# Kernel optimization log

Measured on AMD Instinct MI355X. Metric: run time of the kernel, lower is better.

## Reference

```python
import jax, jax.numpy as jnp
import numpy as np

SOS = 1  # start-of-sequence token id (module references a global SOS)
VOCAB, EMBED, HIDDEN = 32000, 512, 1024

def setup_inputs() -> dict:
    key = jax.random.key(0)
    ks = jax.random.split(key, 8)
    B = 32
    s = lambda k, shape, scale: jax.random.normal(k, shape, dtype=jnp.float32) * scale
    return {
        "init_hidden": s(ks[0], (1, B, HIDDEN), 1.0),
        "encoder_outputs": s(ks[1], (B, 64, HIDDEN), 1.0),
        "tgt_len": 64,
        "embedding": s(ks[2], (VOCAB, EMBED), 1.0),
        "w_ih": s(ks[3], (3 * HIDDEN, EMBED), 0.03),
        "b_ih": s(ks[4], (3 * HIDDEN,), 0.03),
        "w_hh": s(ks[5], (3 * HIDDEN, HIDDEN), 0.03),
        "b_hh": s(ks[6], (3 * HIDDEN,), 0.03),
        "w_out": s(ks[7], (VOCAB, HIDDEN), 0.03),
        "b_out": jnp.zeros((VOCAB,), dtype=jnp.float32),
    }

def reference(init_hidden, encoder_outputs, tgt_len, embedding, w_ih, b_ih, w_hh, b_hh, w_out, b_out):
    B = init_hidden.shape[1]
    h0 = init_hidden[0]                       # [B, H] (num_layers=1)
    tok0 = jnp.full((B,), SOS, dtype=jnp.int32)

    def step(carry, _):
        h, tok = carry
        x = jnp.tanh(embedding[tok])          # [B, E]
        gi = x @ w_ih.T + b_ih                # [B, 3H]
        gh = h @ w_hh.T + b_hh                # [B, 3H]
        i_r, i_z, i_n = jnp.split(gi, 3, axis=-1)
        h_r, h_z, h_n = jnp.split(gh, 3, axis=-1)
        r = jax.nn.sigmoid(i_r + h_r)
        z = jax.nn.sigmoid(i_z + h_z)
        n = jnp.tanh(i_n + r * h_n)
        h_new = (1.0 - z) * n + z * h         # [B, H]
        logp = jax.nn.log_softmax(h_new @ w_out.T + b_out, axis=-1)  # [B, V]
        tok_new = jnp.argmax(logp, axis=-1).astype(jnp.int32)
        return (h_new, tok_new), logp

    (_, _), outputs = jax.lax.scan(step, (h0, tok0), None, length=tgt_len)
    return outputs                            # [T, B, V] log-probs (matches list of squeezed outputs)
```

## Files before the change

kernel.cpp:

```cpp
#include <hip/hip_runtime.h>
#include <math.h>

#define B    32
#define H    1024
#define EMB  512
#define V    32000
#define SOS  1

#define OFF_X   0
#define OFF_HA  16384
#define OFF_HB  49152
#define OFF_P   81920
#define OFF_C   113920
#define OFF_HHI 115968
#define OFF_HLO 132352
#define OFF_WHI 148736
#define OFF_WLO 16532736

#define NEG_INF (-3.0e38f)

typedef float f4v   __attribute__((ext_vector_type(4)));
typedef short short8v __attribute__((ext_vector_type(8)));
typedef float f32x4 __attribute__((ext_vector_type(4)));

#define MF(a,b,c) c = __builtin_amdgcn_mfma_f32_16x16x32_bf16(a, b, c, 0, 0, 0)

__device__ __forceinline__ unsigned short rnb(float x) {
    unsigned u = __float_as_uint(x);
    unsigned r = u + 0x7FFFu + ((u >> 16) & 1u);
    return (unsigned short)(r >> 16);
}
__device__ __forceinline__ float bfh(unsigned short s) {
    return __uint_as_float(((unsigned)s) << 16);
}
__device__ __forceinline__ void sm_merge(float& m, float& l, int& a,
                                         float om, float ol, int oa)
{
    const bool take = (om > m) || (om == m && oa < a);
    const float mn = take ? om : m;
    const int   an = take ? oa : a;
    l = l * expf(m - mn) + ol * expf(om - mn);
    m = mn; a = an;
}

__global__ void k_init(const float* __restrict__ ih, const float* __restrict__ emb,
                       const float* __restrict__ wout, float* __restrict__ ws)
{
    const size_t idx = (size_t)blockIdx.x * blockDim.x + threadIdx.x;
    const size_t stride = (size_t)gridDim.x * blockDim.x;
    for (size_t i = idx; i < EMB * B; i += stride)
        ws[OFF_X + i] = tanhf(emb[(size_t)SOS * EMB + (i >> 5)]);
    for (size_t i = idx; i < H * B; i += stride) {
        int j = (int)(i >> 5), b = (int)(i & 31);
        ws[OFF_HA + j * 32 + b] = ih[(size_t)b * H + j];
    }
    short* Whi = (short*)(ws + OFF_WHI);
    short* Wlo = (short*)(ws + OFF_WLO);
    for (size_t i = idx; i < (size_t)V * H; i += stride) {
        const float x = wout[i];
        const unsigned short hi = rnb(x);
        Whi[i] = (short)hi;
        Wlo[i] = (short)rnb(x - bfh(hi));
    }
}

__global__ __launch_bounds__(1024) void k_gru(
    const float* __restrict__ xG, const float* __restrict__ hold,
    const float* __restrict__ wih, const float* __restrict__ bih,
    const float* __restrict__ whh, const float* __restrict__ bhh,
    float* __restrict__ hnew, short* __restrict__ Hhi, short* __restrict__ Hlo)
{
    const int t   = threadIdx.x;
    const int blk = blockIdx.x;
    __shared__ float sred[4 * 1152];

    const int ks = t >> 7;
    const int pl = t & 127;
    const int p  = blk * 128 + pl;
    const int b  = p & 31;
    const int j  = p >> 5;

    float ar = 0.f, az = 0.f, ain = 0.f, ahn = 0.f;
    const int k0 = ks * 192, k1 = k0 + 192;

    const int xe = (k1 < EMB) ? k1 : EMB;
    for (int k = k0; k < xe; k += 4) {
        const float u0 = xG[(k + 0) * 32 + b];
        const float u1 = xG[(k + 1) * 32 + b];
        const float u2 = xG[(k + 2) * 32 + b];
        const float u3 = xG[(k + 3) * 32 + b];
        const float4 w0 = *(const float4*)&wih[(size_t)(0 * H + j) * EMB + k];
        const float4 w1 = *(const float4*)&wih[(size_t)(1 * H + j) * EMB + k];
        const float4 w2 = *(const float4*)&wih[(size_t)(2 * H + j) * EMB + k];
        ar  = fmaf(w0.x, u0, fmaf(w0.y, u1, fmaf(w0.z, u2, fmaf(w0.w, u3, ar))));
        az  = fmaf(w1.x, u0, fmaf(w1.y, u1, fmaf(w1.z, u2, fmaf(w1.w, u3, az))));
        ain = fmaf(w2.x, u0, fmaf(w2.y, u1, fmaf(w2.z, u2, fmaf(w2.w, u3, ain))));
    }
    const int hs = (k0 > EMB) ? k0 : EMB;
    for (int k = hs; k < k1; k += 4) {
        const int kh = k - EMB;
        const float u0 = hold[(kh + 0) * 32 + b];
        const float u1 = hold[(kh + 1) * 32 + b];
        const float u2 = hold[(kh + 2) * 32 + b];
        const float u3 = hold[(kh + 3) * 32 + b];
        const float4 w0 = *(const float4*)&whh[(size_t)(0 * H + j) * H + kh];
        const float4 w1 = *(const float4*)&whh[(size_t)(1 * H + j) * H + kh];
        const float4 w2 = *(const float4*)&whh[(size_t)(2 * H + j) * H + kh];
        ar  = fmaf(w0.x, u0, fmaf(w0.y, u1, fmaf(w0.z, u2, fmaf(w0.w, u3, ar))));
        az  = fmaf(w1.x, u0, fmaf(w1.y, u1, fmaf(w1.z, u2, fmaf(w1.w, u3, az))));
        ahn = fmaf(w2.x, u0, fmaf(w2.y, u1, fmaf(w2.z, u2, fmaf(w2.w, u3, ahn))));
    }

    sred[0 * 1152 + pl * 9 + ks] = ar;
    sred[1 * 1152 + pl * 9 + ks] = az;
    sred[2 * 1152 + pl * 9 + ks] = ain;
    sred[3 * 1152 + pl * 9 + ks] = ahn;
    __syncthreads();

    if (t < 128) {
        const int pp = blk * 128 + t;
        const int bb = pp & 31, jj = pp >> 5;
        float s0 = 0.f, s1 = 0.f, s2 = 0.f, s3 = 0.f;
#pragma unroll
        for (int q = 0; q < 8; ++q) {
            s0 += sred[0 * 1152 + t * 9 + q];
            s1 += sred[1 * 1152 + t * 9 + q];
            s2 += sred[2 * 1152 + t * 9 + q];
            s3 += sred[3 * 1152 + t * 9 + q];
        }
        float gr  = s0 + bih[jj]         + bhh[jj];
        float gz  = s1 + bih[H + jj]     + bhh[H + jj];
        float gin = s2 + bih[2 * H + jj];
        float ghn = s3 + bhh[2 * H + jj];
        float r = 1.f / (1.f + expf(-gr));
        float z = 1.f / (1.f + expf(-gz));
        float n = tanhf(gin + r * ghn);
        const int hidx = jj * 32 + bb;
        const float hv = (1.f - z) * n + z * hold[hidx];
        hnew[hidx] = hv;
        const unsigned short hi = rnb(hv);
        const unsigned short lo = rnb(hv - bfh(hi));
        const int pidx = (((jj >> 3) * 32) + bb) * 8 + (jj & 7);
        Hhi[pidx] = (short)hi;
        Hlo[pidx] = (short)lo;
    }
}

__global__ __launch_bounds__(256) void k_proj(
    const short* __restrict__ Whi, const short* __restrict__ Wlo,
    const short* __restrict__ Hhi, const short* __restrict__ Hlo,
    const float* __restrict__ bout, float* __restrict__ orow,
    float4* __restrict__ P)
{
    __shared__ float Dt[32 * 132];
    __shared__ float bl[128];
    __shared__ float pm[4][32], pls[4][32];
    __shared__ int   pa[4][32];

    const int t   = threadIdx.x;
    const int blk = blockIdx.x;
    const int r0  = blk * 128;
    const int w   = t >> 6;
    const int l   = t & 63;
    const int lr  = l & 15;
    const int lg  = l >> 4;

    if (t < 128) bl[t] = bout[r0 + t];

    const short* pAh = Whi + (size_t)(r0 + w * 32 + lr) * H + lg * 8;
    const short* pAl = Wlo + (size_t)(r0 + w * 32 + lr) * H + lg * 8;
    const short* pBh = Hhi + (lg * 32 + lr) * 8;
    const short* pBl = Hlo + (lg * 32 + lr) * 8;

    f32x4 acc00 = {0.f, 0.f, 0.f, 0.f};
    f32x4 acc01 = {0.f, 0.f, 0.f, 0.f};
    f32x4 acc10 = {0.f, 0.f, 0.f, 0.f};
    f32x4 acc11 = {0.f, 0.f, 0.f, 0.f};

#pragma unroll 4
    for (int c = 0; c < 32; ++c) {
        const short8v a0h = *(const short8v*)(pAh + c * 32);
        const short8v a1h = *(const short8v*)(pAh + 16 * H + c * 32);
        const short8v a0l = *(const short8v*)(pAl + c * 32);
        const short8v a1l = *(const short8v*)(pAl + 16 * H + c * 32);
        const short8v b0h = *(const short8v*)(pBh + c * 1024);
        const short8v b1h = *(const short8v*)(pBh + c * 1024 + 128);
        const short8v b0l = *(const short8v*)(pBl + c * 1024);
        const short8v b1l = *(const short8v*)(pBl + c * 1024 + 128);
        MF(a0h, b0h, acc00); MF(a0h, b0l, acc00); MF(a0l, b0h, acc00); MF(a0l, b0l, acc00);
        MF(a0h, b1h, acc01); MF(a0h, b1l, acc01); MF(a0l, b1h, acc01); MF(a0l, b1l, acc01);
        MF(a1h, b0h, acc10); MF(a1h, b0l, acc10); MF(a1l, b0h, acc10); MF(a1l, b0l, acc10);
        MF(a1h, b1h, acc11); MF(a1h, b1l, acc11); MF(a1l, b1h, acc11); MF(a1l, b1l, acc11);
    }

    __syncthreads();

    float val[2][2][4];
#pragma unroll
    for (int mt = 0; mt < 2; ++mt)
#pragma unroll
        for (int r = 0; r < 4; ++r) {
            const float bo = bl[w * 32 + mt * 16 + 4 * lg + r];
            val[mt][0][r] = (mt ? acc10[r] : acc00[r]) + bo;
            val[mt][1][r] = (mt ? acc11[r] : acc01[r]) + bo;
        }
#pragma unroll
    for (int mt = 0; mt < 2; ++mt)
#pragma unroll
        for (int nt = 0; nt < 2; ++nt)
#pragma unroll
            for (int r = 0; r < 4; ++r)
                Dt[(nt * 16 + lr) * 132 + w * 32 + mt * 16 + 4 * lg + r] = val[mt][nt][r];

#pragma unroll
    for (int nt = 0; nt < 2; ++nt) {
        float m = val[0][nt][0], lsum = 1.f;
        int   a = r0 + w * 32 + 4 * lg;
#pragma unroll
        for (int q = 1; q < 8; ++q) {
            const int mt = q >> 2, r = q & 3;
            const float x = val[mt][nt][r];
            const int row = r0 + w * 32 + mt * 16 + 4 * lg + r;
            if (x > m) { lsum = lsum * expf(m - x) + 1.f; m = x; a = row; }
            else       { lsum += expf(x - m); }
        }
        sm_merge(m, lsum, a, __shfl_xor(m, 16), __shfl_xor(lsum, 16), __shfl_xor(a, 16));
        sm_merge(m, lsum, a, __shfl_xor(m, 32), __shfl_xor(lsum, 32), __shfl_xor(a, 32));
        if (lg == 0) { pm[w][nt * 16 + lr] = m; pls[w][nt * 16 + lr] = lsum; pa[w][nt * 16 + lr] = a; }
    }
    __syncthreads();

    if (t < 32) {
        float m = pm[0][t], ls = pls[0][t]; int a = pa[0][t];
#pragma unroll
        for (int q = 1; q < 4; ++q) sm_merge(m, ls, a, pm[q][t], pls[q][t], pa[q][t]);
        P[blk * 32 + t] = make_float4(m, ls, (float)a, 0.f);
    }

    const int sb = t >> 3, rq = t & 7;
#pragma unroll
    for (int i = 0; i < 4; ++i) {
        const f4v v = *(const f4v*)&Dt[sb * 132 + rq * 16 + i * 4];
        __builtin_nontemporal_store(v, (f4v*)&orow[(size_t)sb * V + r0 + rq * 16 + i * 4]);
    }
}

__global__ __launch_bounds__(256) void k_fin2(
    const float4* __restrict__ partial, const float* __restrict__ emb,
    float* __restrict__ xG, float* __restrict__ C)
{
    const int b = blockIdx.x;
    const int t = threadIdx.x;
    __shared__ float fm[256], fl[256];
    __shared__ int   fa[256], stok;

    float m = NEG_INF, l = 0.f; int a = 0x7FFFFFFF;
    if (t < 250) {
        float4 p = partial[t * 32 + b];
        m = p.x; l = p.y; a = (int)p.z;
    }
    fm[t] = m; fl[t] = l; fa[t] = a;
    __syncthreads();
    for (int s = 128; s > 0; s >>= 1) {
        if (t < s) {
            const float om = fm[t + s], ol = fl[t + s];
            const int   oa = fa[t + s];
            float mm = fm[t]; float ll = fl[t]; int aa = fa[t];
            const bool take = (om > mm) || (om == mm && oa < aa);
            const float mn = take ? om : mm;
            const int   an = take ? oa : aa;
            ll = ll * expf(mm - mn) + ol * expf(om - mn);
            fm[t] = mn; fl[t] = ll; fa[t] = an;
        }
        __syncthreads();
    }
    if (t == 0) {
        C[b] = fm[0] + logf(fl[0]);
        stok = fa[0];
    }
    __syncthreads();
    const int TOK = stok;
    for (int k = t; k < EMB; k += 256)
        xG[k * 32 + b] = tanhf(emb[(size_t)TOK * EMB + k]);
}

__global__ __launch_bounds__(256) void k_sub(float* __restrict__ out,
                                             const float* __restrict__ C)
{
    const int r = blockIdx.x;
    const float c = C[r];
    f4v* row = (f4v*)(out + (size_t)r * V);
    for (int v = threadIdx.x; v < V / 4; v += 256) {
        f4v x = __builtin_nontemporal_load(&row[v]);
        x -= c;
        __builtin_nontemporal_store(x, &row[v]);
    }
}

extern "C" void kernel_launch(void* const* d_in, const int* in_sizes, int n_in,
                              void* d_out, int out_size, void* d_ws, size_t ws_size,
                              hipStream_t stream)
{
    const float* p_ih   = (const float*)d_in[0];
    const float* p_emb  = (const float*)d_in[3];
    const float* p_wih  = (const float*)d_in[4];
    const float* p_bih  = (const float*)d_in[5];
    const float* p_whh  = (const float*)d_in[6];
    const float* p_bhh  = (const float*)d_in[7];
    const float* p_wout = (const float*)d_in[8];
    const float* p_bout = (const float*)d_in[9];
    float* out = (float*)d_out;
    float* ws  = (float*)d_ws;
    const int T = out_size / (B * V);

    float*  xG  = ws + OFF_X;
    float*  hA  = ws + OFF_HA;
    float*  hB  = ws + OFF_HB;
    float4* P   = (float4*)(ws + OFF_P);
    float*  C   = ws + OFF_C;
    short*  Hhi = (short*)(ws + OFF_HHI);
    short*  Hlo = (short*)(ws + OFF_HLO);
    short*  Whi = (short*)(ws + OFF_WHI);
    short*  Wlo = (short*)(ws + OFF_WLO);

    k_init<<<2048, 256, 0, stream>>>(p_ih, p_emb, p_wout, ws);

    for (int st = 0; st < T; ++st) {
        float* hold = (st & 1) ? hB : hA;
        float* hnew = (st & 1) ? hA : hB;
        float* orow = out + (size_t)st * B * V;
        k_gru<<<256, 1024, 0, stream>>>(xG, hold, p_wih, p_bih, p_whh, p_bhh,
                                        hnew, Hhi, Hlo);
        k_proj<<<250, 256, 0, stream>>>(Whi, Wlo, Hhi, Hlo, p_bout, orow, P);
        k_fin2<<<B, 256, 0, stream>>>(P, p_emb, xG, C + st * B);
    }
    k_sub<<<T * B, 256, 0, stream>>>(out, C);
}
```

Measured before the change: 4.050 ms.

## Split projection into smaller tiles over more blocks, drop lo*lo MFMA term

```diff
diff --git a/kernel.cpp b/kernel.cpp
--- a/kernel.cpp
+++ b/kernel.cpp
@@ -11,11 +11,11 @@
 #define OFF_HA  16384
 #define OFF_HB  49152
 #define OFF_P   81920
-#define OFF_C   113920
-#define OFF_HHI 115968
-#define OFF_HLO 132352
-#define OFF_WHI 148736
-#define OFF_WLO 16532736
+#define OFF_C   145920
+#define OFF_HHI 147968
+#define OFF_HLO 164352
+#define OFF_WHI 180736
+#define OFF_WLO 16564736
 
 #define NEG_INF (-3.0e38f)
 
@@ -146,87 +146,76 @@
     }
 }
 
-__global__ __launch_bounds__(256) void k_proj(
+__global__ __launch_bounds__(512) void k_proj(
     const short* __restrict__ Whi, const short* __restrict__ Wlo,
     const short* __restrict__ Hhi, const short* __restrict__ Hlo,
     const float* __restrict__ bout, float* __restrict__ orow,
     float4* __restrict__ P)
 {
-    __shared__ float Dt[32 * 132];
-    __shared__ float bl[128];
+    __shared__ float Dt[32 * 68];
+    __shared__ float bl[64];
     __shared__ float pm[4][32], pls[4][32];
     __shared__ int   pa[4][32];
 
     const int t   = threadIdx.x;
     const int blk = blockIdx.x;
-    const int r0  = blk * 128;
+    const int r0  = blk * 64;
     const int w   = t >> 6;
+    const int m0  = w >> 1;
+    const int nt  = w & 1;
     const int l   = t & 63;
     const int lr  = l & 15;
     const int lg  = l >> 4;
 
-    if (t < 128) bl[t] = bout[r0 + t];
-
-    const short* pAh = Whi + (size_t)(r0 + w * 32 + lr) * H + lg * 8;
-    const short* pAl = Wlo + (size_t)(r0 + w * 32 + lr) * H + lg * 8;
-    const short* pBh = Hhi + (lg * 32 + lr) * 8;
-    const short* pBl = Hlo + (lg * 32 + lr) * 8;
-
-    f32x4 acc00 = {0.f, 0.f, 0.f, 0.f};
-    f32x4 acc01 = {0.f, 0.f, 0.f, 0.f};
-    f32x4 acc10 = {0.f, 0.f, 0.f, 0.f};
-    f32x4 acc11 = {0.f, 0.f, 0.f, 0.f};
+    if (t < 64) bl[t] = bout[r0 + t];
+
+    const short* pAh = Whi + (size_t)(r0 + m0 * 16 + lr) * H + lg * 8;
+    const short* pAl = Wlo + (size_t)(r0 + m0 * 16 + lr) * H + lg * 8;
+    const short* pBh = Hhi + ((size_t)lg * 32 + nt * 16 + lr) * 8;
+    const short* pBl = Hlo + ((size_t)lg * 32 + nt * 16 + lr) * 8;
+
+    f32x4 accE = {0.f, 0.f, 0.f, 0.f};
+    f32x4 accO = {0.f, 0.f, 0.f, 0.f};
 
 #pragma unroll 4
-    for (int c = 0; c < 32; ++c) {
-        const short8v a0h = *(const short8v*)(pAh + c * 32);
-        const short8v a1h = *(const short8v*)(pAh + 16 * H + c * 32);
-        const short8v a0l = *(const short8v*)(pAl + c * 32);
-        const short8v a1l = *(const short8v*)(pAl + 16 * H + c * 32);
-        const short8v b0h = *(const short8v*)(pBh + c * 1024);
-        const short8v b1h = *(const short8v*)(pBh + c * 1024 + 128);
-        const short8v b0l = *(const short8v*)(pBl + c * 1024);
-        const short8v b1l = *(const short8v*)(pBl + c * 1024 + 128);
-        MF(a0h, b0h, acc00); MF(a0h, b0l, acc00); MF(a0l, b0h, acc00); MF(a0l, b0l, acc00);
-        MF(a0h, b1h, acc01); MF(a0h, b1l, acc01); MF(a0l, b1h, acc01); MF(a0l, b1l, acc01);
-        MF(a1h, b0h, acc10); MF(a1h, b0l, acc10); MF(a1l, b0h, acc10); MF(a1l, b0l, acc10);
-        MF(a1h, b1h, acc11); MF(a1h, b1l, acc11); MF(a1l, b1h, acc11); MF(a1l, b1l, acc11);
-    }
-
-    __syncthreads();
-
-    float val[2][2][4];
-#pragma unroll
-    for (int mt = 0; mt < 2; ++mt)
-#pragma unroll
-        for (int r = 0; r < 4; ++r) {
-            const float bo = bl[w * 32 + mt * 16 + 4 * lg + r];
-            val[mt][0][r] = (mt ? acc10[r] : acc00[r]) + bo;
-            val[mt][1][r] = (mt ? acc11[r] : acc01[r]) + bo;
+    for (int c = 0; c < 32; c += 2) {
+        const short8v aEh = *(const short8v*)(pAh + c * 32);
+        const short8v aEl = *(const short8v*)(pAl + c * 32);
+        const short8v bEh = *(const short8v*)(pBh + c * 1024);
+        const short8v bEl = *(const short8v*)(pBl + c * 1024);
+        const short8v aOh = *(const short8v*)(pAh + (c + 1) * 32);
+        const short8v aOl = *(const short8v*)(pAl + (c + 1) * 32);
+        const short8v bOh = *(const short8v*)(pBh + (c + 1) * 1024);
+        const short8v bOl = *(const short8v*)(pBl + (c + 1) * 1024);
+        MF(aEh, bEh, accE); MF(aEh, bEl, accE); MF(aEl, bEh, accE);
+        MF(aOh, bOh, accO); MF(aOh, bOl, accO); MF(aOl, bOh, accO);
+    }
+
+    __syncthreads();
+
+    const int rowbase = m0 * 16 + 4 * lg;
+    const int bcol    = nt * 16 + lr;
+    float val[4];
+#pragma unroll
+    for (int r = 0; r < 4; ++r)
+        val[r] = accE[r] + accO[r] + bl[rowbase + r];
+
+#pragma unroll
+    for (int r = 0; r < 4; ++r)
+        Dt[bcol * 68 + rowbase + r] = val[r];
+
+    {
+        float m = val[0], ls = 1.f; int a = r0 + rowbase;
+#pragma unroll
+        for (int r = 1; r < 4; ++r) {
+            const float x = val[r];
+            const int row = r0 + rowbase + r;
+            if (x > m) { ls = ls * expf(m - x) + 1.f; m = x; a = row; }
+            else       { ls += expf(x - m); }
         }
-#pragma unroll
-    for (int mt = 0; mt < 2; ++mt)
-#pragma unroll
-        for (int nt = 0; nt < 2; ++nt)
-#pragma unroll
-            for (int r = 0; r < 4; ++r)
-                Dt[(nt * 16 + lr) * 132 + w * 32 + mt * 16 + 4 * lg + r] = val[mt][nt][r];
-
-#pragma unroll
-    for (int nt = 0; nt < 2; ++nt) {
-        float m = val[0][nt][0], lsum = 1.f;
-        int   a = r0 + w * 32 + 4 * lg;
-#pragma unroll
-        for (int q = 1; q < 8; ++q) {
-            const int mt = q >> 2, r = q & 3;
-            const float x = val[mt][nt][r];
-            const int row = r0 + w * 32 + mt * 16 + 4 * lg + r;
-            if (x > m) { lsum = lsum * expf(m - x) + 1.f; m = x; a = row; }
-            else       { lsum += expf(x - m); }
-        }
-        sm_merge(m, lsum, a, __shfl_xor(m, 16), __shfl_xor(lsum, 16), __shfl_xor(a, 16));
-        sm_merge(m, lsum, a, __shfl_xor(m, 32), __shfl_xor(lsum, 32), __shfl_xor(a, 32));
-        if (lg == 0) { pm[w][nt * 16 + lr] = m; pls[w][nt * 16 + lr] = lsum; pa[w][nt * 16 + lr] = a; }
+        sm_merge(m, ls, a, __shfl_xor(m, 16), __shfl_xor(ls, 16), __shfl_xor(a, 16));
+        sm_merge(m, ls, a, __shfl_xor(m, 32), __shfl_xor(ls, 32), __shfl_xor(a, 32));
+        if (lg == 0) { pm[m0][bcol] = m; pls[m0][bcol] = ls; pa[m0][bcol] = a; }
     }
     __syncthreads();
 
@@ -237,12 +226,9 @@
         P[blk * 32 + t] = make_float4(m, ls, (float)a, 0.f);
     }
 
-    const int sb = t >> 3, rq = t & 7;
-#pragma unroll
-    for (int i = 0; i < 4; ++i) {
-        const f4v v = *(const f4v*)&Dt[sb * 132 + rq * 16 + i * 4];
-        __builtin_nontemporal_store(v, (f4v*)&orow[(size_t)sb * V + r0 + rq * 16 + i * 4]);
-    }
+    const int sb = t >> 4, rq = t & 15;
+    const f4v v = *(const f4v*)&Dt[sb * 68 + rq * 4];
+    __builtin_nontemporal_store(v, (f4v*)&orow[(size_t)sb * V + r0 + rq * 4]);
 }
 
 __global__ __launch_bounds__(256) void k_fin2(
@@ -255,9 +241,13 @@
     __shared__ int   fa[256], stok;
 
     float m = NEG_INF, l = 0.f; int a = 0x7FFFFFFF;
-    if (t < 250) {
+    {
         float4 p = partial[t * 32 + b];
         m = p.x; l = p.y; a = (int)p.z;
+    }
+    if (t + 256 < 500) {
+        float4 p = partial[(t + 256) * 32 + b];
+        sm_merge(m, l, a, p.x, p.y, (int)p.z);
     }
     fm[t] = m; fl[t] = l; fa[t] = a;
     __syncthreads();
@@ -331,7 +321,7 @@
         float* orow = out + (size_t)st * B * V;
         k_gru<<<256, 1024, 0, stream>>>(xG, hold, p_wih, p_bih, p_whh, p_bhh,
                                         hnew, Hhi, Hlo);
-        k_proj<<<250, 256, 0, stream>>>(Whi, Wlo, Hhi, Hlo, p_bout, orow, P);
+        k_proj<<<500, 512, 0, stream>>>(Whi, Wlo, Hhi, Hlo, p_bout, orow, P);
         k_fin2<<<B, 256, 0, stream>>>(P, p_emb, xG, C + st * B);
     }
     k_sub<<<T * B, 256, 0, stream>>>(out, C);
```

Result: slower. 4.563 ms (+12.7%).

## Split vocab projection into 64-row blocks with split-K and drop lo*lo MFMA

Applied to the files above, without the earlier changes.

```diff
diff --git a/kernel.cpp b/kernel.cpp
--- a/kernel.cpp
+++ b/kernel.cpp
@@ -11,11 +11,11 @@
 #define OFF_HA  16384
 #define OFF_HB  49152
 #define OFF_P   81920
-#define OFF_C   113920
-#define OFF_HHI 115968
-#define OFF_HLO 132352
-#define OFF_WHI 148736
-#define OFF_WLO 16532736
+#define OFF_C   145920
+#define OFF_HHI 147968
+#define OFF_HLO 164352
+#define OFF_WHI 180736
+#define OFF_WLO 16564736
 
 #define NEG_INF (-3.0e38f)
 
@@ -146,31 +146,34 @@
     }
 }
 
-__global__ __launch_bounds__(256) void k_proj(
+__global__ __launch_bounds__(256, 2) void k_proj(
     const short* __restrict__ Whi, const short* __restrict__ Wlo,
     const short* __restrict__ Hhi, const short* __restrict__ Hlo,
     const float* __restrict__ bout, float* __restrict__ orow,
     float4* __restrict__ P)
 {
-    __shared__ float Dt[32 * 132];
-    __shared__ float bl[128];
-    __shared__ float pm[4][32], pls[4][32];
-    __shared__ int   pa[4][32];
+    __shared__ float Red[2 * 32 * 33];
+    __shared__ float Dt[32 * 68];
+    __shared__ float bl[64];
+    __shared__ float pm[2][32], pls[2][32];
+    __shared__ int   pa[2][32];
 
     const int t   = threadIdx.x;
     const int blk = blockIdx.x;
-    const int r0  = blk * 128;
+    const int r0  = blk * 64;
     const int w   = t >> 6;
+    const int mh  = w >> 1;
+    const int kq  = w & 1;
     const int l   = t & 63;
     const int lr  = l & 15;
     const int lg  = l >> 4;
 
-    if (t < 128) bl[t] = bout[r0 + t];
-
-    const short* pAh = Whi + (size_t)(r0 + w * 32 + lr) * H + lg * 8;
-    const short* pAl = Wlo + (size_t)(r0 + w * 32 + lr) * H + lg * 8;
-    const short* pBh = Hhi + (lg * 32 + lr) * 8;
-    const short* pBl = Hlo + (lg * 32 + lr) * 8;
+    if (t < 64) bl[t] = bout[r0 + t];
+
+    const short* pAh = Whi + (size_t)(r0 + mh * 32 + lr) * H + lg * 8;
+    const short* pAl = Wlo + (size_t)(r0 + mh * 32 + lr) * H + lg * 8;
+    const short* pBh = Hhi + ((size_t)lg * 32 + lr) * 8;
+    const short* pBl = Hlo + ((size_t)lg * 32 + lr) * 8;
 
     f32x4 acc00 = {0.f, 0.f, 0.f, 0.f};
     f32x4 acc01 = {0.f, 0.f, 0.f, 0.f};
@@ -178,70 +181,94 @@
     f32x4 acc11 = {0.f, 0.f, 0.f, 0.f};
 
 #pragma unroll 4
-    for (int c = 0; c < 32; ++c) {
+    for (int i = 0; i < 16; ++i) {
+        const int c = 2 * i + kq;
         const short8v a0h = *(const short8v*)(pAh + c * 32);
+        const short8v a0l = *(const short8v*)(pAl + c * 32);
         const short8v a1h = *(const short8v*)(pAh + 16 * H + c * 32);
-        const short8v a0l = *(const short8v*)(pAl + c * 32);
         const short8v a1l = *(const short8v*)(pAl + 16 * H + c * 32);
         const short8v b0h = *(const short8v*)(pBh + c * 1024);
+        const short8v b0l = *(const short8v*)(pBl + c * 1024);
         const short8v b1h = *(const short8v*)(pBh + c * 1024 + 128);
-        const short8v b0l = *(const short8v*)(pBl + c * 1024);
         const short8v b1l = *(const short8v*)(pBl + c * 1024 + 128);
-        MF(a0h, b0h, acc00); MF(a0h, b0l, acc00); MF(a0l, b0h, acc00); MF(a0l, b0l, acc00);
-        MF(a0h, b1h, acc01); MF(a0h, b1l, acc01); MF(a0l, b1h, acc01); MF(a0l, b1l, acc01);
-        MF(a1h, b0h, acc10); MF(a1h, b0l, acc10); MF(a1l, b0h, acc10); MF(a1l, b0l, acc10);
-        MF(a1h, b1h, acc11); MF(a1h, b1l, acc11); MF(a1l, b1h, acc11); MF(a1l, b1l, acc11);
-    }
-
-    __syncthreads();
-
-    float val[2][2][4];
-#pragma unroll
-    for (int mt = 0; mt < 2; ++mt)
-#pragma unroll
-        for (int r = 0; r < 4; ++r) {
-            const float bo = bl[w * 32 + mt * 16 + 4 * lg + r];
-            val[mt][0][r] = (mt ? acc10[r] : acc00[r]) + bo;
-            val[mt][1][r] = (mt ? acc11[r] : acc01[r]) + bo;
+        MF(a0h, b0h, acc00); MF(a0h, b0l, acc00); MF(a0l, b0h, acc00);
+        MF(a0h, b1h, acc01); MF(a0h, b1l, acc01); MF(a0l, b1h, acc01);
+        MF(a1h, b0h, acc10); MF(a1h, b0l, acc10); MF(a1l, b0h, acc10);
+        MF(a1h, b1h, acc11); MF(a1h, b1l, acc11); MF(a1l, b1h, acc11);
+    }
+
+    if (kq == 1) {
+#pragma unroll
+        for (int mt = 0; mt < 2; ++mt)
+#pragma unroll
+            for (int r = 0; r < 4; ++r) {
+                const int row = mt * 16 + lg * 4 + r;
+                Red[mh * 1056 + row * 33 + lr]      = mt ? acc10[r] : acc00[r];
+                Red[mh * 1056 + row * 33 + 16 + lr] = mt ? acc11[r] : acc01[r];
+            }
+    }
+    __syncthreads();
+
+    if (kq == 0) {
+#pragma unroll
+        for (int mt = 0; mt < 2; ++mt)
+#pragma unroll
+            for (int r = 0; r < 4; ++r) {
+                const int row = mt * 16 + lg * 4 + r;
+                const float e0 = Red[mh * 1056 + row * 33 + lr];
+                const float e1 = Red[mh * 1056 + row * 33 + 16 + lr];
+                if (mt) { acc10[r] += e0; acc11[r] += e1; }
+                else    { acc00[r] += e0; acc01[r] += e1; }
+            }
+
+        float val[2][2][4];
+#pragma unroll
+        for (int mt = 0; mt < 2; ++mt)
+#pragma unroll
+            for (int r = 0; r < 4; ++r) {
+                const float bo = bl[mh * 32 + mt * 16 + lg * 4 + r];
+                val[mt][0][r] = (mt ? acc10[r] : acc00[r]) + bo;
+                val[mt][1][r] = (mt ? acc11[r] : acc01[r]) + bo;
+            }
+#pragma unroll
+        for (int mt = 0; mt < 2; ++mt)
+#pragma unroll
+            for (int nt = 0; nt < 2; ++nt)
+#pragma unroll
+                for (int r = 0; r < 4; ++r)
+                    Dt[(nt * 16 + lr) * 68 + mh * 32 + mt * 16 + lg * 4 + r] = val[mt][nt][r];
+
+#pragma unroll
+        for (int nt = 0; nt < 2; ++nt) {
+            float m = val[0][nt][0], ls = 1.f;
+            int a = r0 + mh * 32 + lg * 4;
+#pragma unroll
+            for (int q = 1; q < 8; ++q) {
+                const int mt = q >> 2, r = q & 3;
+                const float x = val[mt][nt][r];
+                const int row = r0 + mh * 32 + mt * 16 + lg * 4 + r;
+                if (x > m) { ls = ls * expf(m - x) + 1.f; m = x; a = row; }
+                else       { ls += expf(x - m); }
+            }
+            sm_merge(m, ls, a, __shfl_xor(m, 16), __shfl_xor(ls, 16), __shfl_xor(a, 16));
+            sm_merge(m, ls, a, __shfl_xor(m, 32), __shfl_xor(ls, 32), __shfl_xor(a, 32));
+            if (lg == 0) { pm[mh][nt * 16 + lr] = m; pls[mh][nt * 16 + lr] = ls; pa[mh][nt * 16 + lr] = a; }
         }
-#pragma unroll
-    for (int mt = 0; mt < 2; ++mt)
-#pragma unroll
-        for (int nt = 0; nt < 2; ++nt)
-#pragma unroll
-            for (int r = 0; r < 4; ++r)
-                Dt[(nt * 16 + lr) * 132 + w * 32 + mt * 16 + 4 * lg + r] = val[mt][nt][r];
-
-#pragma unroll
-    for (int nt = 0; nt < 2; ++nt) {
-        float m = val[0][nt][0], lsum = 1.f;
-        int   a = r0 + w * 32 + 4 * lg;
-#pragma unroll
-        for (int q = 1; q < 8; ++q) {
-            const int mt = q >> 2, r = q & 3;
-            const float x = val[mt][nt][r];
-            const int row = r0 + w * 32 + mt * 16 + 4 * lg + r;
-            if (x > m) { lsum = lsum * expf(m - x) + 1.f; m = x; a = row; }
-            else       { lsum += expf(x - m); }
-        }
-        sm_merge(m, lsum, a, __shfl_xor(m, 16), __shfl_xor(lsum, 16), __shfl_xor(a, 16));
-        sm_merge(m, lsum, a, __shfl_xor(m, 32), __shfl_xor(lsum, 32), __shfl_xor(a, 32));
-        if (lg == 0) { pm[w][nt * 16 + lr] = m; pls[w][nt * 16 + lr] = lsum; pa[w][nt * 16 + lr] = a; }
     }
     __syncthreads();
 
     if (t < 32) {
         float m = pm[0][t], ls = pls[0][t]; int a = pa[0][t];
-#pragma unroll
-        for (int q = 1; q < 4; ++q) sm_merge(m, ls, a, pm[q][t], pls[q][t], pa[q][t]);
+        sm_merge(m, ls, a, pm[1][t], pls[1][t], pa[1][t]);
         P[blk * 32 + t] = make_float4(m, ls, (float)a, 0.f);
     }
 
     const int sb = t >> 3, rq = t & 7;
 #pragma unroll
-    for (int i = 0; i < 4; ++i) {
-        const f4v v = *(const f4v*)&Dt[sb * 132 + rq * 16 + i * 4];
-        __builtin_nontemporal_store(v, (f4v*)&orow[(size_t)sb * V + r0 + rq * 16 + i * 4]);
+    for (int hx = 0; hx < 2; ++hx) {
+        const f4v v = *(const f4v*)&Dt[sb * 68 + hx * 32 + rq * 4];
+        __builtin_nontemporal_store(v,
+            (f4v*)&orow[(size_t)sb * V + r0 + hx * 32 + rq * 4]);
     }
 }
 
@@ -255,9 +282,13 @@
     __shared__ int   fa[256], stok;
 
     float m = NEG_INF, l = 0.f; int a = 0x7FFFFFFF;
-    if (t < 250) {
+    {
         float4 p = partial[t * 32 + b];
         m = p.x; l = p.y; a = (int)p.z;
+    }
+    if (t + 256 < 500) {
+        float4 p = partial[(t + 256) * 32 + b];
+        sm_merge(m, l, a, p.x, p.y, (int)p.z);
     }
     fm[t] = m; fl[t] = l; fa[t] = a;
     __syncthreads();
@@ -331,7 +362,7 @@
         float* orow = out + (size_t)st * B * V;
         k_gru<<<256, 1024, 0, stream>>>(xG, hold, p_wih, p_bih, p_whh, p_bhh,
                                         hnew, Hhi, Hlo);
-        k_proj<<<250, 256, 0, stream>>>(Whi, Wlo, Hhi, Hlo, p_bout, orow, P);
+        k_proj<<<500, 256, 0, stream>>>(Whi, Wlo, Hhi, Hlo, p_bout, orow, P);
         k_fin2<<<B, 256, 0, stream>>>(P, p_emb, xG, C + st * B);
     }
     k_sub<<<T * B, 256, 0, stream>>>(out, C);
```

After: 3.776 ms. 6.8% less time.
